# Kernel tuning notes

Hardware: AMD Instinct MI355X
Metric: run time of the kernel (lower is better)

## Reference

```python
import jax, jax.numpy as jnp
import numpy as np

BETA = 0.25


def setup_inputs() -> dict:
    key = jax.random.key(0)
    k1, k2 = jax.random.split(key)
    x = jax.random.normal(k1, (32, 64, 64, 64), dtype=jnp.float32)
    # tf.random_uniform_initializer default: uniform in [-0.05, 0.05]
    embeddings = jax.random.uniform(k2, (64, 512), dtype=jnp.float32, minval=-0.05, maxval=0.05)
    return {"x": x, "embeddings": embeddings}


def reference(x, embeddings):
    D = embeddings.shape[0]
    flat = x.reshape(-1, D)  # [N, D]
    # squared euclidean distances via the matmul expansion: [N, K]
    distances = (
        jnp.sum(flat * flat, axis=1, keepdims=True)
        - 2.0 * (flat @ embeddings)
        + jnp.sum(embeddings * embeddings, axis=0, keepdims=True)
    )
    codes = jnp.argmin(distances, axis=1)  # [N]
    # direct gather of codebook rows (math-equivalent to one_hot @ embeddings.T)
    quantized = embeddings.T[codes].reshape(x.shape)
    loss = (
        jnp.mean((jax.lax.stop_gradient(x) - quantized) ** 2)
        + BETA * jnp.mean((x - jax.lax.stop_gradient(quantized)) ** 2)
    )
    # straight-through estimator
    out = x + jax.lax.stop_gradient(quantized - x)
    return out, loss
```

## Files before the change

### kernel.cpp

```cpp
#include <hip/hip_runtime.h>
#include <cstddef>

#define D 64
#define K 512
#define NROWS (32*64*64)
#define RPB 64
#define NBLK (NROWS / RPB)
#define NOUT 8388608


__global__ __launch_bounds__(256) void vq_prep(const float* __restrict__ emb,
                                               float* __restrict__ eT,
                                               float* __restrict__ enorm) {
    const int k = blockIdx.x * blockDim.x + threadIdx.x;
    if (k >= K) return;
    float nrm = 0.f;
#pragma unroll
    for (int d = 0; d < D; ++d) {
        const float v = emb[d * K + k];
        nrm = __fadd_rn(nrm, __fmul_rn(v, v));
        eT[k * D + d] = v;
    }
    enorm[k] = nrm;
}

__global__ __launch_bounds__(256, 4) void vq_main(const float* __restrict__ x,
                                                  const float* __restrict__ eT,
                                                  const float* __restrict__ enorm,
                                                  float* __restrict__ out,
                                                  float* __restrict__ partials) {
    __shared__ float s_dist[256];
    __shared__ int   s_idx[256];
    __shared__ int   s_code[RPB];
    __shared__ float s_red[4];

    const int t    = threadIdx.x;
    const int wave = t >> 6;
    const int lane = t & 63;
    const size_t rowbase = (size_t)blockIdx.x * RPB;
    const size_t row = rowbase + lane;

    float xr[64];
    const float4* __restrict__ xv = (const float4*)(x + row * D);
#pragma unroll
    for (int j = 0; j < 16; ++j) {
        const float4 v = xv[j];
        xr[4*j+0] = v.x; xr[4*j+1] = v.y; xr[4*j+2] = v.z; xr[4*j+3] = v.w;
    }
#pragma unroll
    for (int j = 0; j < 16; ++j) {
        asm volatile("" : "+v"(xr[4*j+0]), "+v"(xr[4*j+1]),
                          "+v"(xr[4*j+2]), "+v"(xr[4*j+3]));
    }

    float r0 = __fmul_rn(xr[0], xr[0]), r1 = __fmul_rn(xr[1], xr[1]);
    float r2 = __fmul_rn(xr[2], xr[2]), r3 = __fmul_rn(xr[3], xr[3]);
    float r4 = __fmul_rn(xr[4], xr[4]), r5 = __fmul_rn(xr[5], xr[5]);
    float r6 = __fmul_rn(xr[6], xr[6]), r7 = __fmul_rn(xr[7], xr[7]);
#pragma unroll
    for (int b = 1; b < 8; ++b) {
        r0 = __fadd_rn(r0, __fmul_rn(xr[8*b+0], xr[8*b+0]));
        r1 = __fadd_rn(r1, __fmul_rn(xr[8*b+1], xr[8*b+1]));
        r2 = __fadd_rn(r2, __fmul_rn(xr[8*b+2], xr[8*b+2]));
        r3 = __fadd_rn(r3, __fmul_rn(xr[8*b+3], xr[8*b+3]));
        r4 = __fadd_rn(r4, __fmul_rn(xr[8*b+4], xr[8*b+4]));
        r5 = __fadd_rn(r5, __fmul_rn(xr[8*b+5], xr[8*b+5]));
        r6 = __fadd_rn(r6, __fmul_rn(xr[8*b+6], xr[8*b+6]));
        r7 = __fadd_rn(r7, __fmul_rn(xr[8*b+7], xr[8*b+7]));
    }
    const float xnorm = __fadd_rn(__fadd_rn(__fadd_rn(r0, r1), __fadd_rn(r2, r3)),
                                  __fadd_rn(__fadd_rn(r4, r5), __fadd_rn(r6, r7)));

    const int kbase = __builtin_amdgcn_readfirstlane(wave << 7);
    float best = 3.4028235e38f;
    int   bidx = 0;
    for (int kk = 0; kk < 128; kk += 4) {
        const float4* __restrict__ e0 = (const float4*)(eT + (size_t)(kbase + kk + 0) * D);
        const float4* __restrict__ e1 = (const float4*)(eT + (size_t)(kbase + kk + 1) * D);
        const float4* __restrict__ e2 = (const float4*)(eT + (size_t)(kbase + kk + 2) * D);
        const float4* __restrict__ e3 = (const float4*)(eT + (size_t)(kbase + kk + 3) * D);
        float a00 = 0.f, a01 = 0.f, a02 = 0.f, a03 = 0.f;
        float a10 = 0.f, a11 = 0.f, a12 = 0.f, a13 = 0.f;
        float a20 = 0.f, a21 = 0.f, a22 = 0.f, a23 = 0.f;
        float a30 = 0.f, a31 = 0.f, a32 = 0.f, a33 = 0.f;
#pragma unroll
        for (int j = 0; j < 16; ++j) {
            const float4 v0 = e0[j], v1 = e1[j], v2 = e2[j], v3 = e3[j];
            const float x0 = xr[4*j+0], x1 = xr[4*j+1], x2 = xr[4*j+2], x3 = xr[4*j+3];
            a00 = fmaf(x0, v0.x, a00); a10 = fmaf(x0, v1.x, a10); a20 = fmaf(x0, v2.x, a20); a30 = fmaf(x0, v3.x, a30);
            a01 = fmaf(x1, v0.y, a01); a11 = fmaf(x1, v1.y, a11); a21 = fmaf(x1, v2.y, a21); a31 = fmaf(x1, v3.y, a31);
            a02 = fmaf(x2, v0.z, a02); a12 = fmaf(x2, v1.z, a12); a22 = fmaf(x2, v2.z, a22); a32 = fmaf(x2, v3.z, a32);
            a03 = fmaf(x3, v0.w, a03); a13 = fmaf(x3, v1.w, a13); a23 = fmaf(x3, v2.w, a23); a33 = fmaf(x3, v3.w, a33);
        }
        const float dot0 = __fadd_rn(__fadd_rn(a00, a01), __fadd_rn(a02, a03));
        const float dot1 = __fadd_rn(__fadd_rn(a10, a11), __fadd_rn(a12, a13));
        const float dot2 = __fadd_rn(__fadd_rn(a20, a21), __fadd_rn(a22, a23));
        const float dot3 = __fadd_rn(__fadd_rn(a30, a31), __fadd_rn(a32, a33));
        const float d0 = __fadd_rn(__fsub_rn(xnorm, __fmul_rn(2.f, dot0)), enorm[kbase + kk + 0]);
        const float d1 = __fadd_rn(__fsub_rn(xnorm, __fmul_rn(2.f, dot1)), enorm[kbase + kk + 1]);
        const float d2 = __fadd_rn(__fsub_rn(xnorm, __fmul_rn(2.f, dot2)), enorm[kbase + kk + 2]);
        const float d3 = __fadd_rn(__fsub_rn(xnorm, __fmul_rn(2.f, dot3)), enorm[kbase + kk + 3]);
        if (d0 < best) { best = d0; bidx = kbase + kk + 0; }
        if (d1 < best) { best = d1; bidx = kbase + kk + 1; }
        if (d2 < best) { best = d2; bidx = kbase + kk + 2; }
        if (d3 < best) { best = d3; bidx = kbase + kk + 3; }
    }

    s_dist[t] = best;
    s_idx[t]  = bidx;
    __syncthreads();
    if (t < RPB) {
        float bb = s_dist[t];
        int   bi = s_idx[t];
#pragma unroll
        for (int w = 1; w < 4; ++w) {
            const float ob = s_dist[w * 64 + t];
            const int   oi = s_idx[w * 64 + t];
            if (ob < bb) { bb = ob; bi = oi; }
        }
        s_code[t] = bi;
    }
    __syncthreads();

    const int c  = t & 15;
    const int r0i = t >> 4;
    float lacc = 0.f;
#pragma unroll
    for (int i = 0; i < 4; ++i) {
        const int r = r0i + 16 * i;
        const int code = s_code[r];
        const float4 q = *(const float4*)(eT + (size_t)code * D + 4 * c);
        const float4 b = *(const float4*)(x + (rowbase + r) * D + 4 * c);
        const float f0 = __fsub_rn(b.x, q.x), f1 = __fsub_rn(b.y, q.y);
        const float f2 = __fsub_rn(b.z, q.z), f3 = __fsub_rn(b.w, q.w);
        lacc = fmaf(f0, f0, lacc); lacc = fmaf(f1, f1, lacc);
        lacc = fmaf(f2, f2, lacc); lacc = fmaf(f3, f3, lacc);
        float4 o;
        o.x = __fadd_rn(b.x, __fsub_rn(q.x, b.x));
        o.y = __fadd_rn(b.y, __fsub_rn(q.y, b.y));
        o.z = __fadd_rn(b.z, __fsub_rn(q.z, b.z));
        o.w = __fadd_rn(b.w, __fsub_rn(q.w, b.w));
        *(float4*)(out + (rowbase + r) * D + 4 * c) = o;
    }

#pragma unroll
    for (int off = 32; off > 0; off >>= 1) lacc += __shfl_down(lacc, off);
    if (lane == 0) s_red[wave] = lacc;
    __syncthreads();
    if (t == 0) partials[blockIdx.x] = (s_red[0] + s_red[1]) + (s_red[2] + s_red[3]);
}

__global__ __launch_bounds__(256) void vq_finish(const float* __restrict__ partials,
                                                 float* __restrict__ loss_out) {
    __shared__ float s_red[4];
    const int t = threadIdx.x;
    float a = 0.f;
#pragma unroll
    for (int i = 0; i < 8; ++i) a += partials[t + 256 * i];
#pragma unroll
    for (int off = 32; off > 0; off >>= 1) a += __shfl_down(a, off);
    if ((t & 63) == 0) s_red[t >> 6] = a;
    __syncthreads();
    if (t == 0) {
        const float S = (s_red[0] + s_red[1]) + (s_red[2] + s_red[3]);
        const float m = S / (float)NOUT;
        loss_out[0] = m + 0.25f * m;
    }
}

extern "C" void kernel_launch(void* const* d_in, const int* in_sizes, int n_in,
                              void* d_out, int out_size, void* d_ws, size_t ws_size,
                              hipStream_t stream) {
    const float* x   = (const float*)d_in[0];
    const float* emb = (const float*)d_in[1];
    float* out = (float*)d_out;
    float* ws  = (float*)d_ws;

    float* eT       = ws;
    float* enorm    = ws + 32768;
    float* partials = ws + 32768 + 512;

    vq_prep<<<2, 256, 0, stream>>>(emb, eT, enorm);
    vq_main<<<NBLK, 256, 0, stream>>>(x, eT, enorm, out, partials);
    vq_finish<<<1, 256, 0, stream>>>(partials, out + NOUT);
}
```

Baseline: 221.1 us.

## Stage codebook chunks into LDS with async double-buffered global_load_lds

```diff
diff --git a/kernel.cpp b/kernel.cpp
--- a/kernel.cpp
+++ b/kernel.cpp
@@ -4,9 +4,14 @@
 #define D 64
 #define K 512
 #define NROWS (32*64*64)
-#define RPB 64
+#define RPB 128
 #define NBLK (NROWS / RPB)
 #define NOUT 8388608
+#define CHUNK 16
+#define NCHUNK 16
+
+typedef __attribute__((address_space(1))) const void glb_cvoid;
+typedef __attribute__((address_space(3))) void lds_void;
 
 
 __global__ __launch_bounds__(256) void vq_prep(const float* __restrict__ emb,
@@ -29,6 +34,7 @@
                                                   const float* __restrict__ enorm,
                                                   float* __restrict__ out,
                                                   float* __restrict__ partials) {
+    __shared__ float s_ebuf[4][2][CHUNK * D];
     __shared__ float s_dist[256];
     __shared__ int   s_idx[256];
     __shared__ int   s_code[RPB];
@@ -37,8 +43,11 @@
     const int t    = threadIdx.x;
     const int wave = t >> 6;
     const int lane = t & 63;
+    const int rg   = wave >> 1;
+    const int kh   = wave & 1;
     const size_t rowbase = (size_t)blockIdx.x * RPB;
-    const size_t row = rowbase + lane;
+    const int    rl  = (rg << 6) + lane;
+    const size_t row = rowbase + rl;
 
     float xr[64];
     const float4* __restrict__ xv = (const float4*)(x + row * D);
@@ -52,6 +61,21 @@
         asm volatile("" : "+v"(xr[4*j+0]), "+v"(xr[4*j+1]),
                           "+v"(xr[4*j+2]), "+v"(xr[4*j+3]));
     }
+
+    const int kbase = kh << 8;
+    const float* __restrict__ esrc = eT + (size_t)kbase * D;
+    float* const edst0 = &s_ebuf[wave][0][0];
+    float* const edst1 = &s_ebuf[wave][1][0];
+
+    auto stage = [&](float* dst, int c) {
+        const float* src = esrc + (size_t)c * (CHUNK * D) + (lane << 2);
+#pragma unroll
+        for (int i = 0; i < 4; ++i) {
+            __builtin_amdgcn_global_load_lds((glb_cvoid*)(src + i * 256),
+                                             (lds_void*)(dst + i * 256), 16, 0, 0);
+        }
+    };
+    stage(edst0, 0);
 
     float r0 = __fmul_rn(xr[0], xr[0]), r1 = __fmul_rn(xr[1], xr[1]);
     float r2 = __fmul_rn(xr[2], xr[2]), r3 = __fmul_rn(xr[3], xr[3]);
@@ -71,66 +95,65 @@
     const float xnorm = __fadd_rn(__fadd_rn(__fadd_rn(r0, r1), __fadd_rn(r2, r3)),
                                   __fadd_rn(__fadd_rn(r4, r5), __fadd_rn(r6, r7)));
 
-    const int kbase = __builtin_amdgcn_readfirstlane(wave << 7);
     float best = 3.4028235e38f;
     int   bidx = 0;
-    for (int kk = 0; kk < 128; kk += 4) {
-        const float4* __restrict__ e0 = (const float4*)(eT + (size_t)(kbase + kk + 0) * D);
-        const float4* __restrict__ e1 = (const float4*)(eT + (size_t)(kbase + kk + 1) * D);
-        const float4* __restrict__ e2 = (const float4*)(eT + (size_t)(kbase + kk + 2) * D);
-        const float4* __restrict__ e3 = (const float4*)(eT + (size_t)(kbase + kk + 3) * D);
-        float a00 = 0.f, a01 = 0.f, a02 = 0.f, a03 = 0.f;
-        float a10 = 0.f, a11 = 0.f, a12 = 0.f, a13 = 0.f;
-        float a20 = 0.f, a21 = 0.f, a22 = 0.f, a23 = 0.f;
-        float a30 = 0.f, a31 = 0.f, a32 = 0.f, a33 = 0.f;
-#pragma unroll
-        for (int j = 0; j < 16; ++j) {
-            const float4 v0 = e0[j], v1 = e1[j], v2 = e2[j], v3 = e3[j];
-            const float x0 = xr[4*j+0], x1 = xr[4*j+1], x2 = xr[4*j+2], x3 = xr[4*j+3];
-            a00 = fmaf(x0, v0.x, a00); a10 = fmaf(x0, v1.x, a10); a20 = fmaf(x0, v2.x, a20); a30 = fmaf(x0, v3.x, a30);
-            a01 = fmaf(x1, v0.y, a01); a11 = fmaf(x1, v1.y, a11); a21 = fmaf(x1, v2.y, a21); a31 = fmaf(x1, v3.y, a31);
-            a02 = fmaf(x2, v0.z, a02); a12 = fmaf(x2, v1.z, a12); a22 = fmaf(x2, v2.z, a22); a32 = fmaf(x2, v3.z, a32);
-            a03 = fmaf(x3, v0.w, a03); a13 = fmaf(x3, v1.w, a13); a23 = fmaf(x3, v2.w, a23); a33 = fmaf(x3, v3.w, a33);
+#pragma unroll 1
+    for (int c = 0; c < NCHUNK; ++c) {
+        const float* eb = (c & 1) ? edst1 : edst0;
+        if (c + 1 < NCHUNK) {
+            stage((c & 1) ? edst0 : edst1, c + 1);
+            asm volatile("s_waitcnt vmcnt(4)" ::: "memory");
+        } else {
+            asm volatile("s_waitcnt vmcnt(0)" ::: "memory");
         }
-        const float dot0 = __fadd_rn(__fadd_rn(a00, a01), __fadd_rn(a02, a03));
-        const float dot1 = __fadd_rn(__fadd_rn(a10, a11), __fadd_rn(a12, a13));
-        const float dot2 = __fadd_rn(__fadd_rn(a20, a21), __fadd_rn(a22, a23));
-        const float dot3 = __fadd_rn(__fadd_rn(a30, a31), __fadd_rn(a32, a33));
-        const float d0 = __fadd_rn(__fsub_rn(xnorm, __fmul_rn(2.f, dot0)), enorm[kbase + kk + 0]);
-        const float d1 = __fadd_rn(__fsub_rn(xnorm, __fmul_rn(2.f, dot1)), enorm[kbase + kk + 1]);
-        const float d2 = __fadd_rn(__fsub_rn(xnorm, __fmul_rn(2.f, dot2)), enorm[kbase + kk + 2]);
-        const float d3 = __fadd_rn(__fsub_rn(xnorm, __fmul_rn(2.f, dot3)), enorm[kbase + kk + 3]);
-        if (d0 < best) { best = d0; bidx = kbase + kk + 0; }
-        if (d1 < best) { best = d1; bidx = kbase + kk + 1; }
-        if (d2 < best) { best = d2; bidx = kbase + kk + 2; }
-        if (d3 < best) { best = d3; bidx = kbase + kk + 3; }
+        __builtin_amdgcn_sched_barrier(0);
+        const int kc = kbase + c * CHUNK;
+#pragma unroll 1
+        for (int g = 0; g < CHUNK / 2; ++g) {
+            const float4* __restrict__ e0 = (const float4*)(eb + (2*g+0) * D);
+            const float4* __restrict__ e1 = (const float4*)(eb + (2*g+1) * D);
+            float a00 = 0.f, a01 = 0.f, a02 = 0.f, a03 = 0.f;
+            float a10 = 0.f, a11 = 0.f, a12 = 0.f, a13 = 0.f;
+#pragma unroll
+            for (int j = 0; j < 16; ++j) {
+                const float4 v0 = e0[j], v1 = e1[j];
+                const float x0 = xr[4*j+0], x1 = xr[4*j+1];
+                const float x2 = xr[4*j+2], x3 = xr[4*j+3];
+                a00 = fmaf(x0, v0.x, a00); a10 = fmaf(x0, v1.x, a10);
+                a01 = fmaf(x1, v0.y, a01); a11 = fmaf(x1, v1.y, a11);
+                a02 = fmaf(x2, v0.z, a02); a12 = fmaf(x2, v1.z, a12);
+                a03 = fmaf(x3, v0.w, a03); a13 = fmaf(x3, v1.w, a13);
+            }
+            const float dot0 = __fadd_rn(__fadd_rn(a00, a01), __fadd_rn(a02, a03));
+            const float dot1 = __fadd_rn(__fadd_rn(a10, a11), __fadd_rn(a12, a13));
+            const float d0 = __fadd_rn(__fsub_rn(xnorm, __fmul_rn(2.f, dot0)), enorm[kc + 2*g + 0]);
+            const float d1 = __fadd_rn(__fsub_rn(xnorm, __fmul_rn(2.f, dot1)), enorm[kc + 2*g + 1]);
+            if (d0 < best) { best = d0; bidx = kc + 2*g + 0; }
+            if (d1 < best) { best = d1; bidx = kc + 2*g + 1; }
+        }
     }
 
     s_dist[t] = best;
     s_idx[t]  = bidx;
     __syncthreads();
     if (t < RPB) {
-        float bb = s_dist[t];
-        int   bi = s_idx[t];
-#pragma unroll
-        for (int w = 1; w < 4; ++w) {
-            const float ob = s_dist[w * 64 + t];
-            const int   oi = s_idx[w * 64 + t];
-            if (ob < bb) { bb = ob; bi = oi; }
-        }
-        s_code[t] = bi;
-    }
-    __syncthreads();
-
-    const int c  = t & 15;
+        const int t0 = ((t >> 6) << 7) + (t & 63);
+        float b0 = s_dist[t0];      int i0 = s_idx[t0];
+        const float b1 = s_dist[t0 + 64]; const int i1 = s_idx[t0 + 64];
+        if (b1 < b0) { b0 = b1; i0 = i1; }
+        s_code[t] = i0;
+    }
+    __syncthreads();
+
+    const int cch = t & 15;
     const int r0i = t >> 4;
     float lacc = 0.f;
 #pragma unroll
-    for (int i = 0; i < 4; ++i) {
+    for (int i = 0; i < 8; ++i) {
         const int r = r0i + 16 * i;
         const int code = s_code[r];
-        const float4 q = *(const float4*)(eT + (size_t)code * D + 4 * c);
-        const float4 b = *(const float4*)(x + (rowbase + r) * D + 4 * c);
+        const float4 q = *(const float4*)(eT + (size_t)code * D + 4 * cch);
+        const float4 b = *(const float4*)(x + (rowbase + r) * D + 4 * cch);
         const float f0 = __fsub_rn(b.x, q.x), f1 = __fsub_rn(b.y, q.y);
         const float f2 = __fsub_rn(b.z, q.z), f3 = __fsub_rn(b.w, q.w);
         lacc = fmaf(f0, f0, lacc); lacc = fmaf(f1, f1, lacc);
@@ -140,7 +163,7 @@
         o.y = __fadd_rn(b.y, __fsub_rn(q.y, b.y));
         o.z = __fadd_rn(b.z, __fsub_rn(q.z, b.z));
         o.w = __fadd_rn(b.w, __fsub_rn(q.w, b.w));
-        *(float4*)(out + (rowbase + r) * D + 4 * c) = o;
+        *(float4*)(out + (rowbase + r) * D + 4 * cch) = o;
     }
 
 #pragma unroll
@@ -156,7 +179,7 @@
     const int t = threadIdx.x;
     float a = 0.f;
 #pragma unroll
-    for (int i = 0; i < 8; ++i) a += partials[t + 256 * i];
+    for (int i = 0; i < 4; ++i) a += partials[t + 256 * i];
 #pragma unroll
     for (int off = 32; off > 0; off >>= 1) a += __shfl_down(a, off);
     if ((t & 63) == 0) s_red[t >> 6] = a;
```

After: 265.2 us. 1.2x slower.

## Stage x rows in transposed LDS tile and widen codebook tile to eight codes

Applied to the files above, without the earlier changes.

```diff
diff --git a/kernel.cpp b/kernel.cpp
--- a/kernel.cpp
+++ b/kernel.cpp
@@ -24,11 +24,12 @@
     enorm[k] = nrm;
 }
 
-__global__ __launch_bounds__(256, 4) void vq_main(const float* __restrict__ x,
-                                                  const float* __restrict__ eT,
-                                                  const float* __restrict__ enorm,
-                                                  float* __restrict__ out,
-                                                  float* __restrict__ partials) {
+__global__ __launch_bounds__(256) void vq_main(const float* __restrict__ x,
+                                               const float* __restrict__ eT,
+                                               const float* __restrict__ enorm,
+                                               float* __restrict__ out,
+                                               float* __restrict__ partials) {
+    __shared__ float xT[D][RPB];
     __shared__ float s_dist[256];
     __shared__ int   s_idx[256];
     __shared__ int   s_code[RPB];
@@ -38,35 +39,40 @@
     const int wave = t >> 6;
     const int lane = t & 63;
     const size_t rowbase = (size_t)blockIdx.x * RPB;
-    const size_t row = rowbase + lane;
 
-    float xr[64];
-    const float4* __restrict__ xv = (const float4*)(x + row * D);
+    {
+        const float4* __restrict__ src = (const float4*)(x + (rowbase + lane) * D + wave * 16);
+        const float4 v0 = src[0], v1 = src[1], v2 = src[2], v3 = src[3];
+        const int d0 = wave * 16;
+        xT[d0+ 0][lane] = v0.x; xT[d0+ 1][lane] = v0.y; xT[d0+ 2][lane] = v0.z; xT[d0+ 3][lane] = v0.w;
+        xT[d0+ 4][lane] = v1.x; xT[d0+ 5][lane] = v1.y; xT[d0+ 6][lane] = v1.z; xT[d0+ 7][lane] = v1.w;
+        xT[d0+ 8][lane] = v2.x; xT[d0+ 9][lane] = v2.y; xT[d0+10][lane] = v2.z; xT[d0+11][lane] = v2.w;
+        xT[d0+12][lane] = v3.x; xT[d0+13][lane] = v3.y; xT[d0+14][lane] = v3.z; xT[d0+15][lane] = v3.w;
+    }
+    __syncthreads();
+
+    float r0, r1, r2, r3, r4, r5, r6, r7;
+    {
+        float v;
+        v = xT[0][lane]; r0 = __fmul_rn(v, v);
+        v = xT[1][lane]; r1 = __fmul_rn(v, v);
+        v = xT[2][lane]; r2 = __fmul_rn(v, v);
+        v = xT[3][lane]; r3 = __fmul_rn(v, v);
+        v = xT[4][lane]; r4 = __fmul_rn(v, v);
+        v = xT[5][lane]; r5 = __fmul_rn(v, v);
+        v = xT[6][lane]; r6 = __fmul_rn(v, v);
+        v = xT[7][lane]; r7 = __fmul_rn(v, v);
 #pragma unroll
-    for (int j = 0; j < 16; ++j) {
-        const float4 v = xv[j];
-        xr[4*j+0] = v.x; xr[4*j+1] = v.y; xr[4*j+2] = v.z; xr[4*j+3] = v.w;
-    }
-#pragma unroll
-    for (int j = 0; j < 16; ++j) {
-        asm volatile("" : "+v"(xr[4*j+0]), "+v"(xr[4*j+1]),
-                          "+v"(xr[4*j+2]), "+v"(xr[4*j+3]));
-    }
-
-    float r0 = __fmul_rn(xr[0], xr[0]), r1 = __fmul_rn(xr[1], xr[1]);
-    float r2 = __fmul_rn(xr[2], xr[2]), r3 = __fmul_rn(xr[3], xr[3]);
-    float r4 = __fmul_rn(xr[4], xr[4]), r5 = __fmul_rn(xr[5], xr[5]);
-    float r6 = __fmul_rn(xr[6], xr[6]), r7 = __fmul_rn(xr[7], xr[7]);
-#pragma unroll
-    for (int b = 1; b < 8; ++b) {
-        r0 = __fadd_rn(r0, __fmul_rn(xr[8*b+0], xr[8*b+0]));
-        r1 = __fadd_rn(r1, __fmul_rn(xr[8*b+1], xr[8*b+1]));
-        r2 = __fadd_rn(r2, __fmul_rn(xr[8*b+2], xr[8*b+2]));
-        r3 = __fadd_rn(r3, __fmul_rn(xr[8*b+3], xr[8*b+3]));
-        r4 = __fadd_rn(r4, __fmul_rn(xr[8*b+4], xr[8*b+4]));
-        r5 = __fadd_rn(r5, __fmul_rn(xr[8*b+5], xr[8*b+5]));
-        r6 = __fadd_rn(r6, __fmul_rn(xr[8*b+6], xr[8*b+6]));
-        r7 = __fadd_rn(r7, __fmul_rn(xr[8*b+7], xr[8*b+7]));
+        for (int b = 1; b < 8; ++b) {
+            v = xT[8*b+0][lane]; r0 = __fadd_rn(r0, __fmul_rn(v, v));
+            v = xT[8*b+1][lane]; r1 = __fadd_rn(r1, __fmul_rn(v, v));
+            v = xT[8*b+2][lane]; r2 = __fadd_rn(r2, __fmul_rn(v, v));
+            v = xT[8*b+3][lane]; r3 = __fadd_rn(r3, __fmul_rn(v, v));
+            v = xT[8*b+4][lane]; r4 = __fadd_rn(r4, __fmul_rn(v, v));
+            v = xT[8*b+5][lane]; r5 = __fadd_rn(r5, __fmul_rn(v, v));
+            v = xT[8*b+6][lane]; r6 = __fadd_rn(r6, __fmul_rn(v, v));
+            v = xT[8*b+7][lane]; r7 = __fadd_rn(r7, __fmul_rn(v, v));
+        }
     }
     const float xnorm = __fadd_rn(__fadd_rn(__fadd_rn(r0, r1), __fadd_rn(r2, r3)),
                                   __fadd_rn(__fadd_rn(r4, r5), __fadd_rn(r6, r7)));
@@ -74,36 +80,37 @@
     const int kbase = __builtin_amdgcn_readfirstlane(wave << 7);
     float best = 3.4028235e38f;
     int   bidx = 0;
-    for (int kk = 0; kk < 128; kk += 4) {
-        const float4* __restrict__ e0 = (const float4*)(eT + (size_t)(kbase + kk + 0) * D);
-        const float4* __restrict__ e1 = (const float4*)(eT + (size_t)(kbase + kk + 1) * D);
-        const float4* __restrict__ e2 = (const float4*)(eT + (size_t)(kbase + kk + 2) * D);
-        const float4* __restrict__ e3 = (const float4*)(eT + (size_t)(kbase + kk + 3) * D);
-        float a00 = 0.f, a01 = 0.f, a02 = 0.f, a03 = 0.f;
-        float a10 = 0.f, a11 = 0.f, a12 = 0.f, a13 = 0.f;
-        float a20 = 0.f, a21 = 0.f, a22 = 0.f, a23 = 0.f;
-        float a30 = 0.f, a31 = 0.f, a32 = 0.f, a33 = 0.f;
+#pragma unroll 1
+    for (int g = 0; g < 16; ++g) {
+        const int kc = kbase + g * 8;
+        const float* __restrict__ eg = eT + (size_t)kc * D;
+        float acc[8][4];
+#pragma unroll
+        for (int c = 0; c < 8; ++c) {
+            acc[c][0] = 0.f; acc[c][1] = 0.f; acc[c][2] = 0.f; acc[c][3] = 0.f;
+        }
 #pragma unroll
         for (int j = 0; j < 16; ++j) {
-            const float4 v0 = e0[j], v1 = e1[j], v2 = e2[j], v3 = e3[j];
-            const float x0 = xr[4*j+0], x1 = xr[4*j+1], x2 = xr[4*j+2], x3 = xr[4*j+3];
-            a00 = fmaf(x0, v0.x, a00); a10 = fmaf(x0, v1.x, a10); a20 = fmaf(x0, v2.x, a20); a30 = fmaf(x0, v3.x, a30);
-            a01 = fmaf(x1, v0.y, a01); a11 = fmaf(x1, v1.y, a11); a21 = fmaf(x1, v2.y, a21); a31 = fmaf(x1, v3.y, a31);
-            a02 = fmaf(x2, v0.z, a02); a12 = fmaf(x2, v1.z, a12); a22 = fmaf(x2, v2.z, a22); a32 = fmaf(x2, v3.z, a32);
-            a03 = fmaf(x3, v0.w, a03); a13 = fmaf(x3, v1.w, a13); a23 = fmaf(x3, v2.w, a23); a33 = fmaf(x3, v3.w, a33);
+            const float x0 = xT[4*j+0][lane];
+            const float x1 = xT[4*j+1][lane];
+            const float x2 = xT[4*j+2][lane];
+            const float x3 = xT[4*j+3][lane];
+#pragma unroll
+            for (int c = 0; c < 8; ++c) {
+                const float4 v = *(const float4*)(eg + (size_t)c * D + 4*j);
+                acc[c][0] = fmaf(x0, v.x, acc[c][0]);
+                acc[c][1] = fmaf(x1, v.y, acc[c][1]);
+                acc[c][2] = fmaf(x2, v.z, acc[c][2]);
+                acc[c][3] = fmaf(x3, v.w, acc[c][3]);
+            }
         }
-        const float dot0 = __fadd_rn(__fadd_rn(a00, a01), __fadd_rn(a02, a03));
-        const float dot1 = __fadd_rn(__fadd_rn(a10, a11), __fadd_rn(a12, a13));
-        const float dot2 = __fadd_rn(__fadd_rn(a20, a21), __fadd_rn(a22, a23));
-        const float dot3 = __fadd_rn(__fadd_rn(a30, a31), __fadd_rn(a32, a33));
-        const float d0 = __fadd_rn(__fsub_rn(xnorm, __fmul_rn(2.f, dot0)), enorm[kbase + kk + 0]);
-        const float d1 = __fadd_rn(__fsub_rn(xnorm, __fmul_rn(2.f, dot1)), enorm[kbase + kk + 1]);
-        const float d2 = __fadd_rn(__fsub_rn(xnorm, __fmul_rn(2.f, dot2)), enorm[kbase + kk + 2]);
-        const float d3 = __fadd_rn(__fsub_rn(xnorm, __fmul_rn(2.f, dot3)), enorm[kbase + kk + 3]);
-        if (d0 < best) { best = d0; bidx = kbase + kk + 0; }
-        if (d1 < best) { best = d1; bidx = kbase + kk + 1; }
-        if (d2 < best) { best = d2; bidx = kbase + kk + 2; }
-        if (d3 < best) { best = d3; bidx = kbase + kk + 3; }
+#pragma unroll
+        for (int c = 0; c < 8; ++c) {
+            const float dot = __fadd_rn(__fadd_rn(acc[c][0], acc[c][1]),
+                                        __fadd_rn(acc[c][2], acc[c][3]));
+            const float dd = __fadd_rn(__fsub_rn(xnorm, __fmul_rn(2.f, dot)), enorm[kc + c]);
+            if (dd < best) { best = dd; bidx = kc + c; }
+        }
     }
 
     s_dist[t] = best;
@@ -122,7 +129,7 @@
     }
     __syncthreads();
 
-    const int c  = t & 15;
+    const int c   = t & 15;
     const int r0i = t >> 4;
     float lacc = 0.f;
 #pragma unroll
```

After: 236.4 us. +7.0%, slower.
